# Kernel tuning notes

Hardware: AMD Instinct MI355X
Metric: run time of the kernel (lower is better)

The kernel has to match this reference:

```python
import jax, jax.numpy as jnp
import numpy as np

B, N = 128, 64
HID, MLP, DS, DV = 128, 128, 32, 32
DH = MLP - DS - DV  # 64
FILL = -10.0


def _embed_mask(x, W, b, fill):
    # Linear+ReLU on non-NaN rows; fill NaN rows with `fill` (matches embed_with_masking).
    nan = jnp.isnan(x).any(-1)
    e = jax.nn.relu(jnp.where(jnp.isnan(x), 0.0, x) @ W + b)
    return jnp.where(nan[..., None], jnp.asarray(fill, x.dtype), e)


def setup_inputs() -> dict:
    key = jax.random.key(0)
    ks = jax.random.split(key, 12)
    s = 0.05
    return {
        "hidden_states": jax.random.normal(ks[0], (B, N, HID), jnp.float32),
        "obs1": jax.random.normal(ks[1], (B, N, 2), jnp.float32),
        "obs2": jax.random.normal(ks[2], (B, N, 2), jnp.float32),
        "w_sp": jax.random.normal(ks[3], (2, DS), jnp.float32) * s,
        "b_sp": jnp.zeros((DS,), jnp.float32),
        "w_vel": jax.random.normal(ks[4], (2, DV), jnp.float32) * s,
        "b_vel": jnp.zeros((DV,), jnp.float32),
        "w_hid": jax.random.normal(ks[5], (HID, DH), jnp.float32) * s,
        "b_hid": jnp.zeros((DH,), jnp.float32),
        "wq": jax.random.normal(ks[6], (MLP, MLP), jnp.float32) * s,
        "wk": jax.random.normal(ks[7], (MLP, MLP), jnp.float32) * s,
        "wv": jax.random.normal(ks[8], (MLP, MLP), jnp.float32) * s,
        "in_proj_w": jax.random.normal(ks[9], (MLP, 3 * MLP), jnp.float32) * s,
        "in_proj_b": jnp.zeros((3 * MLP,), jnp.float32),
        "mha_out_w": jax.random.normal(ks[10], (MLP, MLP), jnp.float32) * s,
        "mha_out_b": jnp.zeros((MLP,), jnp.float32),
        "out_w": jax.random.normal(ks[11], (MLP, MLP), jnp.float32) * s,
        "out_b": jnp.zeros((MLP,), jnp.float32),
    }


def reference(hidden_states, obs1, obs2, w_sp, b_sp, w_vel, b_vel, w_hid, b_hid,
              wq, wk, wv, in_proj_w, in_proj_b, mha_out_w, mha_out_b, out_w, out_b):
    b, n = obs2.shape[0], obs2.shape[1]
    # relative positions: rel[b,i,j] = obs2[b,j] - obs2[b,i]
    rel = obs2[:, None, :, :] - obs2[:, :, None, :]              # [B,N,N,2]
    sp = _embed_mask(rel, w_sp, b_sp, FILL)                      # [B,N,N,DS]
    hid = _embed_mask(hidden_states, w_hid, b_hid, 0.0)          # [B,N,DH]
    hid_unf = jnp.broadcast_to(hid[:, None, :, :], (b, n, n, DH))
    vel = obs2 - obs1
    relvel = vel[:, None, :, :] - vel[:, :, None, :]             # [B,N,N,2]
    dv = _embed_mask(relvel * 4, w_vel, b_vel, FILL)             # [B,N,N,DV]
    emb = jnp.concatenate([sp, hid_unf, dv], axis=-1)            # [B,N,N,MLP]

    # MHA (1 head) in-proj weights split (stored as [in,out])
    w_iq, w_ik, w_iv = in_proj_w[:, :MLP], in_proj_w[:, MLP:2 * MLP], in_proj_w[:, 2 * MLP:]
    b_iq, b_ik, b_iv = in_proj_b[:MLP], in_proj_b[MLP:2 * MLP], in_proj_b[2 * MLP:]

    # Only the diagonal query position is kept by the final eye-mask gather,
    # and softmax rows are independent, so compute q only at j == i.
    idx = jnp.arange(n)
    emb_diag = emb[:, idx, idx]                                  # [B,N,MLP]
    q = (emb_diag @ wq) @ w_iq + b_iq                            # [B,N,MLP]
    k = (emb @ wk) @ w_ik + b_ik                                 # [B,N,N,MLP]
    v = (emb @ wv) @ w_iv + b_iv                                 # [B,N,N,MLP]

    scores = jnp.einsum('bid,bijd->bij', q, k) / jnp.sqrt(jnp.asarray(MLP, q.dtype))
    attn = jax.nn.softmax(scores, axis=-1)                       # [B,N,N]
    ctx = jnp.einsum('bij,bijd->bid', attn, v)                   # [B,N,MLP]
    mha_out = ctx @ mha_out_w + mha_out_b
    out = mha_out @ out_w + out_b                                # [B,N,out_dim]
    return out.reshape(b * n, -1)
```

## Files before the change

### kernel.cpp

```cpp
#include <hip/hip_runtime.h>

#define WS_WQC  0
#define WS_WKC  16384
#define WS_WVC  32768
#define WS_MOW  49152
#define WS_G    65536
#define WS_GS   69632
#define WS_GD   71680
#define WS_G0   73728
#define WS_GS0  73792
#define WS_GD0  73824
#define WS_FSP  73856
#define WS_FDV  77952
#define WS_FHID 82048
#define WS_FB   90240

__global__ __launch_bounds__(128) void precompute1(
    const float* __restrict__ wq, const float* __restrict__ wk,
    const float* __restrict__ wv, const float* __restrict__ in_proj_w,
    const float* __restrict__ mha_out_w, const float* __restrict__ out_w,
    float* __restrict__ ws)
{
    __shared__ float arow[128];
    const int mat = blockIdx.x & 3;
    const int r   = blockIdx.x >> 2;
    const int tid = threadIdx.x;
    const float* A; const float* Bm; int ldb; float* C;
    if (mat == 0)      { A = wq;        Bm = in_proj_w;       ldb = 384; C = ws + WS_WQC; }
    else if (mat == 1) { A = wk;        Bm = in_proj_w + 128; ldb = 384; C = ws + WS_WKC; }
    else if (mat == 2) { A = wv;        Bm = in_proj_w + 256; ldb = 384; C = ws + WS_WVC; }
    else               { A = mha_out_w; Bm = out_w;           ldb = 128; C = ws + WS_MOW; }
    arow[tid] = A[r * 128 + tid];
    __syncthreads();
    float acc = 0.f;
    #pragma unroll 8
    for (int d = 0; d < 128; ++d) acc = fmaf(arow[d], Bm[d * ldb + tid], acc);
    C[r * 128 + tid] = acc;
}

__global__ __launch_bounds__(128) void precompute2(
    const float* __restrict__ b_sp, const float* __restrict__ b_vel,
    const float* __restrict__ in_proj_b, const float* __restrict__ mha_out_b,
    const float* __restrict__ out_w, const float* __restrict__ out_b,
    float* __restrict__ ws)
{
    const float* Wqc = ws + WS_WQC;
    const float* Wkc = ws + WS_WKC;
    const float* Wvc = ws + WS_WVC;
    const float* Mow = ws + WS_MOW;
    const int bid = blockIdx.x, tid = threadIdx.x;
    __shared__ float sa[256];

    if (bid < 64) {
        const int r = bid;
        sa[tid] = Wqc[(32 + r) * 128 + tid];
        __syncthreads();
        const float* brow; float* dst;
        if (tid < 64)      { brow = Wkc + (32 + tid) * 128;      dst = ws + WS_G  + r * 64 + tid; }
        else if (tid < 96) { brow = Wkc + (tid - 64) * 128;      dst = ws + WS_GS + r * 32 + (tid - 64); }
        else               { brow = Wkc + (96 + tid - 96) * 128; dst = ws + WS_GD + r * 32 + (tid - 96); }
        float acc = 0.f;
        #pragma unroll 8
        for (int d = 0; d < 128; ++d) acc = fmaf(sa[d], brow[d], acc);
        *dst = acc;
    } else if (bid < 96) {
        const int s = bid - 64;
        sa[tid]       = Wvc[s * 128 + tid];
        sa[128 + tid] = Wvc[(96 + s) * 128 + tid];
        __syncthreads();
        float a1 = 0.f, a2 = 0.f;
        #pragma unroll 8
        for (int m = 0; m < 128; ++m) {
            const float mo = Mow[m * 128 + tid];
            a1 = fmaf(sa[m], mo, a1);
            a2 = fmaf(sa[128 + m], mo, a2);
        }
        ws[WS_FSP + s * 128 + tid] = a1;
        ws[WS_FDV + s * 128 + tid] = a2;
    } else if (bid < 160) {
        const int c = bid - 96;
        sa[tid] = Wvc[(32 + c) * 128 + tid];
        __syncthreads();
        float acc = 0.f;
        #pragma unroll 8
        for (int m = 0; m < 128; ++m) acc = fmaf(sa[m], Mow[m * 128 + tid], acc);
        ws[WS_FHID + c * 128 + tid] = acc;
    } else if (bid == 160) {
        float acc = out_b[tid];
        #pragma unroll 8
        for (int m = 0; m < 128; ++m) {
            acc = fmaf(in_proj_b[256 + m], Mow[m * 128 + tid], acc);
            acc = fmaf(mha_out_b[m], out_w[m * 128 + tid], acc);
        }
        ws[WS_FB + tid] = acc;
    } else {
        float qc = in_proj_b[tid];
        #pragma unroll 4
        for (int s = 0; s < 32; ++s) {
            qc = fmaf(fmaxf(b_sp[s], 0.f),  Wqc[s * 128 + tid], qc);
            qc = fmaf(fmaxf(b_vel[s], 0.f), Wqc[(96 + s) * 128 + tid], qc);
        }
        sa[tid] = qc;
        __syncthreads();
        const float* brow; float* dst;
        if (tid < 64)      { brow = Wkc + (32 + tid) * 128;      dst = ws + WS_G0  + tid; }
        else if (tid < 96) { brow = Wkc + (tid - 64) * 128;      dst = ws + WS_GS0 + (tid - 64); }
        else               { brow = Wkc + (96 + tid - 96) * 128; dst = ws + WS_GD0 + (tid - 96); }
        float acc = 0.f;
        #pragma unroll 8
        for (int d = 0; d < 128; ++d) acc = fmaf(sa[d], brow[d], acc);
        *dst = acc;
    }
}

__global__ __launch_bounds__(256) void attn_main(
    const float* __restrict__ hs, const float* __restrict__ obs1,
    const float* __restrict__ obs2,
    const float* __restrict__ w_sp, const float* __restrict__ b_sp,
    const float* __restrict__ w_vel, const float* __restrict__ b_vel,
    const float* __restrict__ w_hid, const float* __restrict__ b_hid,
    const float* __restrict__ ws, float* __restrict__ out)
{
    const int tid  = threadIdx.x;
    const int lane = tid & 63;
    const int b    = blockIdx.x >> 1;
    const int i0   = (blockIdx.x & 1) * 32;

    const float* Gm   = ws + WS_G;
    const float* Gs   = ws + WS_GS;
    const float* Gd   = ws + WS_GD;
    const float* g0v  = ws + WS_G0;
    const float* gs0v = ws + WS_GS0;
    const float* gd0v = ws + WS_GD0;
    const float* Fsp  = ws + WS_FSP;
    const float* Fdv  = ws + WS_FDV;
    const float* Fhid = ws + WS_FHID;
    const float* fbv  = ws + WS_FB;

    __shared__ __align__(16) float sA[8192];
    __shared__ __align__(16) float s_hid[4096];
    __shared__ __align__(16) float s_w[192];
    __shared__ __align__(16) float s_obs[256];

    float* const s_t    = sA;
    float* const s_qs   = sA + 2048;
    float* const s_qd   = sA + 3072;
    float* const s_hidT = sA + 4096;
    float* const s_ssp  = sA + 4096;
    float* const s_sdv  = sA + 5120;
    float* const s_ah   = sA + 6144;

    if (tid < 192) {
        float v;
        if (tid < 64)       v = w_sp[tid];
        else if (tid < 128) v = w_vel[tid - 64];
        else if (tid < 160) v = b_sp[tid - 128];
        else                v = b_vel[tid - 160];
        s_w[tid] = v;
    }
    if (tid < 64) {
        const int g = b * 64 + tid;
        const float ox = obs2[g * 2 + 0];
        const float oy = obs2[g * 2 + 1];
        const float vx = ox - obs1[g * 2 + 0];
        const float vy = oy - obs1[g * 2 + 1];
        *(float4*)&s_obs[tid * 4] = make_float4(ox, oy, vx, vy);
    }

    for (int h = 0; h < 2; ++h) {
        const float4* srcH = (const float4*)(hs + b * 8192 + h * 4096);
        float4* dstA = (float4*)sA;
        #pragma unroll
        for (int k = tid; k < 1024; k += 256) dstA[k] = srcH[k];
        __syncthreads();
        {
            const int ty = tid >> 4, tx = tid & 15;
            float a0c[4] = {0,0,0,0}, a1c[4] = {0,0,0,0};
            for (int d0 = 0; d0 < 128; d0 += 4) {
                const float4 a0 = *(const float4*)&sA[(2*ty+0)*128 + d0];
                const float4 a1 = *(const float4*)&sA[(2*ty+1)*128 + d0];
                const float* a0p = (const float*)&a0;
                const float* a1p = (const float*)&a1;
                #pragma unroll
                for (int dd = 0; dd < 4; ++dd) {
                    const float4 w4 = *(const float4*)&w_hid[(d0+dd)*64 + 4*tx];
                    a0c[0] = fmaf(a0p[dd], w4.x, a0c[0]);
                    a0c[1] = fmaf(a0p[dd], w4.y, a0c[1]);
                    a0c[2] = fmaf(a0p[dd], w4.z, a0c[2]);
                    a0c[3] = fmaf(a0p[dd], w4.w, a0c[3]);
                    a1c[0] = fmaf(a1p[dd], w4.x, a1c[0]);
                    a1c[1] = fmaf(a1p[dd], w4.y, a1c[1]);
                    a1c[2] = fmaf(a1p[dd], w4.z, a1c[2]);
                    a1c[3] = fmaf(a1p[dd], w4.w, a1c[3]);
                }
            }
            const float4 bh = *(const float4*)&b_hid[4*tx];
            float v0[4], v1[4];
            v0[0] = fmaxf(a0c[0] + bh.x, 0.f); v0[1] = fmaxf(a0c[1] + bh.y, 0.f);
            v0[2] = fmaxf(a0c[2] + bh.z, 0.f); v0[3] = fmaxf(a0c[3] + bh.w, 0.f);
            v1[0] = fmaxf(a1c[0] + bh.x, 0.f); v1[1] = fmaxf(a1c[1] + bh.y, 0.f);
            v1[2] = fmaxf(a1c[2] + bh.z, 0.f); v1[3] = fmaxf(a1c[3] + bh.w, 0.f);
            const int r0 = 32*h + 2*ty;
            *(float4*)&s_hid[(r0+0)*64 + 4*tx] = make_float4(v0[0], v0[1], v0[2], v0[3]);
            *(float4*)&s_hid[(r0+1)*64 + 4*tx] = make_float4(v1[0], v1[1], v1[2], v1[3]);
            #pragma unroll
            for (int cc = 0; cc < 4; ++cc)
                *(float2*)&s_hidT[(4*tx+cc)*64 + r0] = make_float2(v0[cc], v1[cc]);
        }
        __syncthreads();
    }

    {
        const int ty = tid >> 4, tx = tid & 15;
        const int r0 = i0 + 2*ty;
        {
            const float4 gb = *(const float4*)&g0v[4*tx];
            float t0[4] = {gb.x, gb.y, gb.z, gb.w};
            float t1[4] = {gb.x, gb.y, gb.z, gb.w};
            for (int k0 = 0; k0 < 64; k0 += 4) {
                const float4 a0 = *(const float4*)&s_hid[(r0+0)*64 + k0];
                const float4 a1 = *(const float4*)&s_hid[(r0+1)*64 + k0];
                const float* a0p = (const float*)&a0;
                const float* a1p = (const float*)&a1;
                #pragma unroll
                for (int kk = 0; kk < 4; ++kk) {
                    const float4 g4 = *(const float4*)&Gm[(k0+kk)*64 + 4*tx];
                    t0[0] = fmaf(a0p[kk], g4.x, t0[0]); t0[1] = fmaf(a0p[kk], g4.y, t0[1]);
                    t0[2] = fmaf(a0p[kk], g4.z, t0[2]); t0[3] = fmaf(a0p[kk], g4.w, t0[3]);
                    t1[0] = fmaf(a1p[kk], g4.x, t1[0]); t1[1] = fmaf(a1p[kk], g4.y, t1[1]);
                    t1[2] = fmaf(a1p[kk], g4.z, t1[2]); t1[3] = fmaf(a1p[kk], g4.w, t1[3]);
                }
            }
            *(float4*)&s_t[(2*ty+0)*64 + 4*tx] = make_float4(t0[0], t0[1], t0[2], t0[3]);
            *(float4*)&s_t[(2*ty+1)*64 + 4*tx] = make_float4(t1[0], t1[1], t1[2], t1[3]);
        }
        {
            const float* Bm  = (tx < 8) ? Gs : Gd;
            const float* bm0 = (tx < 8) ? gs0v : gd0v;
            float* dstm      = (tx < 8) ? s_qs : s_qd;
            const int nc = (tx & 7) * 4;
            const float4 bb = *(const float4*)&bm0[nc];
            float q0[4] = {bb.x, bb.y, bb.z, bb.w};
            float q1[4] = {bb.x, bb.y, bb.z, bb.w};
            for (int k0 = 0; k0 < 64; k0 += 4) {
                const float4 a0 = *(const float4*)&s_hid[(r0+0)*64 + k0];
                const float4 a1 = *(const float4*)&s_hid[(r0+1)*64 + k0];
                const float* a0p = (const float*)&a0;
                const float* a1p = (const float*)&a1;
                #pragma unroll
                for (int kk = 0; kk < 4; ++kk) {
                    const float4 g4 = *(const float4*)&Bm[(k0+kk)*32 + nc];
                    q0[0] = fmaf(a0p[kk], g4.x, q0[0]); q0[1] = fmaf(a0p[kk], g4.y, q0[1]);
                    q0[2] = fmaf(a0p[kk], g4.z, q0[2]); q0[3] = fmaf(a0p[kk], g4.w, q0[3]);
                    q1[0] = fmaf(a1p[kk], g4.x, q1[0]); q1[1] = fmaf(a1p[kk], g4.y, q1[1]);
                    q1[2] = fmaf(a1p[kk], g4.z, q1[2]); q1[3] = fmaf(a1p[kk], g4.w, q1[3]);
                }
            }
            *(float4*)&dstm[(2*ty+0)*32 + nc] = make_float4(q0[0], q0[1], q0[2], q0[3]);
            *(float4*)&dstm[(2*ty+1)*32 + nc] = make_float4(q1[0], q1[1], q1[2], q1[3]);
        }
    }
    __syncthreads();

    {
        const int ty = tid >> 4, tx = tid & 15;
        float q0[4] = {0,0,0,0}, q1[4] = {0,0,0,0};
        for (int c0 = 0; c0 < 64; c0 += 4) {
            const float4 t40 = *(const float4*)&s_t[(2*ty+0)*64 + c0];
            const float4 t41 = *(const float4*)&s_t[(2*ty+1)*64 + c0];
            const float* t0p = (const float*)&t40;
            const float* t1p = (const float*)&t41;
            #pragma unroll
            for (int cc = 0; cc < 4; ++cc) {
                const float4 h4 = *(const float4*)&s_hidT[(c0+cc)*64 + 4*tx];
                q0[0] = fmaf(t0p[cc], h4.x, q0[0]); q0[1] = fmaf(t0p[cc], h4.y, q0[1]);
                q0[2] = fmaf(t0p[cc], h4.z, q0[2]); q0[3] = fmaf(t0p[cc], h4.w, q0[3]);
                q1[0] = fmaf(t1p[cc], h4.x, q1[0]); q1[1] = fmaf(t1p[cc], h4.y, q1[1]);
                q1[2] = fmaf(t1p[cc], h4.z, q1[2]); q1[3] = fmaf(t1p[cc], h4.w, q1[3]);
            }
        }
        __syncthreads();
        *(float4*)&s_t[(2*ty+0)*64 + 4*tx] = make_float4(q0[0], q0[1], q0[2], q0[3]);
        *(float4*)&s_t[(2*ty+1)*64 + 4*tx] = make_float4(q1[0], q1[1], q1[2], q1[3]);
    }
    __syncthreads();

    {
        const int wid = tid >> 6;
        float relx[8], rely[8], dvx[8], dvy[8], accr[8];
        const float4 oj = *(const float4*)&s_obs[lane * 4];
        #pragma unroll
        for (int k = 0; k < 8; ++k) {
            const int i = i0 + wid * 8 + k;
            const float4 oi = *(const float4*)&s_obs[i * 4];
            relx[k] = oj.x - oi.x;
            rely[k] = oj.y - oi.y;
            dvx[k]  = (oj.z - oi.z) * 4.f;
            dvy[k]  = (oj.w - oi.w) * 4.f;
            accr[k] = 0.f;
        }
        for (int s0 = 0; s0 < 32; s0 += 4) {
            const float4 w0  = *(const float4*)&s_w[s0];
            const float4 w1  = *(const float4*)&s_w[32 + s0];
            const float4 wv0 = *(const float4*)&s_w[64 + s0];
            const float4 wv1 = *(const float4*)&s_w[96 + s0];
            const float4 bs  = *(const float4*)&s_w[128 + s0];
            const float4 bv  = *(const float4*)&s_w[160 + s0];
            #pragma unroll
            for (int k = 0; k < 8; ++k) {
                const int r = wid * 8 + k;
                const float4 qs4 = *(const float4*)&s_qs[r * 32 + s0];
                const float4 qd4 = *(const float4*)&s_qd[r * 32 + s0];
                float acc = accr[k];
                acc = fmaf(qs4.x, fmaxf(fmaf(relx[k], w0.x, fmaf(rely[k], w1.x, bs.x)), 0.f), acc);
                acc = fmaf(qs4.y, fmaxf(fmaf(relx[k], w0.y, fmaf(rely[k], w1.y, bs.y)), 0.f), acc);
                acc = fmaf(qs4.z, fmaxf(fmaf(relx[k], w0.z, fmaf(rely[k], w1.z, bs.z)), 0.f), acc);
                acc = fmaf(qs4.w, fmaxf(fmaf(relx[k], w0.w, fmaf(rely[k], w1.w, bs.w)), 0.f), acc);
                acc = fmaf(qd4.x, fmaxf(fmaf(dvx[k], wv0.x, fmaf(dvy[k], wv1.x, bv.x)), 0.f), acc);
                acc = fmaf(qd4.y, fmaxf(fmaf(dvx[k], wv0.y, fmaf(dvy[k], wv1.y, bv.y)), 0.f), acc);
                acc = fmaf(qd4.z, fmaxf(fmaf(dvx[k], wv0.z, fmaf(dvy[k], wv1.z, bv.z)), 0.f), acc);
                acc = fmaf(qd4.w, fmaxf(fmaf(dvx[k], wv0.w, fmaf(dvy[k], wv1.w, bv.w)), 0.f), acc);
                accr[k] = acc;
            }
        }
        const float scale = 0.08838834764831845f;
        #pragma unroll
        for (int k = 0; k < 8; ++k) {
            const int r = wid * 8 + k;
            const float sc = (s_t[r * 64 + lane] + accr[k]) * scale;
            float m = sc;
            #pragma unroll
            for (int off = 32; off > 0; off >>= 1) m = fmaxf(m, __shfl_xor(m, off, 64));
            const float e = __expf(sc - m);
            float sum = e;
            #pragma unroll
            for (int off = 32; off > 0; off >>= 1) sum += __shfl_xor(sum, off, 64);
            s_t[r * 64 + lane] = e / sum;
        }
    }
    __syncthreads();

    {
        const int sx = tid & 7, r6 = tid >> 3;
        const int i = i0 + r6;
        const float4 w0  = *(const float4*)&s_w[4*sx];
        const float4 w1  = *(const float4*)&s_w[32 + 4*sx];
        const float4 wv0 = *(const float4*)&s_w[64 + 4*sx];
        const float4 wv1 = *(const float4*)&s_w[96 + 4*sx];
        const float4 bs  = *(const float4*)&s_w[128 + 4*sx];
        const float4 bv  = *(const float4*)&s_w[160 + 4*sx];
        const float4 oi  = *(const float4*)&s_obs[i * 4];
        float sp0=0, sp1=0, sp2=0, sp3=0, dv0=0, dv1=0, dv2=0, dv3=0;
        for (int j0 = 0; j0 < 64; j0 += 4) {
            const float4 at4 = *(const float4*)&s_t[r6 * 64 + j0];
            const float* atp = (const float*)&at4;
            #pragma unroll
            for (int jj = 0; jj < 4; ++jj) {
                const float4 oj4 = *(const float4*)&s_obs[(j0 + jj) * 4];
                const float a  = atp[jj];
                const float rx = oj4.x - oi.x, ry = oj4.y - oi.y;
                const float dx = (oj4.z - oi.z) * 4.f, dy = (oj4.w - oi.w) * 4.f;
                sp0 = fmaf(a, fmaxf(fmaf(rx, w0.x, fmaf(ry, w1.x, bs.x)), 0.f), sp0);
                sp1 = fmaf(a, fmaxf(fmaf(rx, w0.y, fmaf(ry, w1.y, bs.y)), 0.f), sp1);
                sp2 = fmaf(a, fmaxf(fmaf(rx, w0.z, fmaf(ry, w1.z, bs.z)), 0.f), sp2);
                sp3 = fmaf(a, fmaxf(fmaf(rx, w0.w, fmaf(ry, w1.w, bs.w)), 0.f), sp3);
                dv0 = fmaf(a, fmaxf(fmaf(dx, wv0.x, fmaf(dy, wv1.x, bv.x)), 0.f), dv0);
                dv1 = fmaf(a, fmaxf(fmaf(dx, wv0.y, fmaf(dy, wv1.y, bv.y)), 0.f), dv1);
                dv2 = fmaf(a, fmaxf(fmaf(dx, wv0.z, fmaf(dy, wv1.z, bv.z)), 0.f), dv2);
                dv3 = fmaf(a, fmaxf(fmaf(dx, wv0.w, fmaf(dy, wv1.w, bv.w)), 0.f), dv3);
            }
        }
        *(float4*)&s_ssp[r6 * 32 + 4*sx] = make_float4(sp0, sp1, sp2, sp3);
        *(float4*)&s_sdv[r6 * 32 + 4*sx] = make_float4(dv0, dv1, dv2, dv3);

        const int ty = tid >> 4, tx = tid & 15;
        float h0[4] = {0,0,0,0}, h1[4] = {0,0,0,0};
        for (int j0 = 0; j0 < 64; j0 += 4) {
            const float4 at0 = *(const float4*)&s_t[(2*ty+0)*64 + j0];
            const float4 at1 = *(const float4*)&s_t[(2*ty+1)*64 + j0];
            const float* a0p = (const float*)&at0;
            const float* a1p = (const float*)&at1;
            #pragma unroll
            for (int jj = 0; jj < 4; ++jj) {
                const float4 h4 = *(const float4*)&s_hid[(j0+jj)*64 + 4*tx];
                h0[0] = fmaf(a0p[jj], h4.x, h0[0]); h0[1] = fmaf(a0p[jj], h4.y, h0[1]);
                h0[2] = fmaf(a0p[jj], h4.z, h0[2]); h0[3] = fmaf(a0p[jj], h4.w, h0[3]);
                h1[0] = fmaf(a1p[jj], h4.x, h1[0]); h1[1] = fmaf(a1p[jj], h4.y, h1[1]);
                h1[2] = fmaf(a1p[jj], h4.z, h1[2]); h1[3] = fmaf(a1p[jj], h4.w, h1[3]);
            }
        }
        *(float4*)&s_ah[(2*ty+0)*64 + 4*tx] = make_float4(h0[0], h0[1], h0[2], h0[3]);
        *(float4*)&s_ah[(2*ty+1)*64 + 4*tx] = make_float4(h1[0], h1[1], h1[2], h1[3]);
    }
    __syncthreads();

    {
        const int ty = tid >> 4, tx = tid & 15;
        const float4 fba = *(const float4*)&fbv[8*tx];
        const float4 fbb = *(const float4*)&fbv[8*tx + 4];
        float o0a[4] = {fba.x, fba.y, fba.z, fba.w};
        float o0b[4] = {fbb.x, fbb.y, fbb.z, fbb.w};
        float o1a[4] = {fba.x, fba.y, fba.z, fba.w};
        float o1b[4] = {fbb.x, fbb.y, fbb.z, fbb.w};

        #define ACC_TERM(SMAT, LD, FMAT, KMAX)                                        \
        for (int k0 = 0; k0 < (KMAX); k0 += 4) {                                      \
            const float4 a0 = *(const float4*)&SMAT[(2*ty+0)*(LD) + k0];              \
            const float4 a1 = *(const float4*)&SMAT[(2*ty+1)*(LD) + k0];              \
            const float* a0p = (const float*)&a0;                                     \
            const float* a1p = (const float*)&a1;                                     \
            _Pragma("unroll")                                                         \
            for (int kk = 0; kk < 4; ++kk) {                                          \
                const float4 fa = *(const float4*)&FMAT[(k0+kk)*128 + 8*tx];          \
                const float4 fbq = *(const float4*)&FMAT[(k0+kk)*128 + 8*tx + 4];     \
                o0a[0] = fmaf(a0p[kk], fa.x, o0a[0]); o0a[1] = fmaf(a0p[kk], fa.y, o0a[1]); \
                o0a[2] = fmaf(a0p[kk], fa.z, o0a[2]); o0a[3] = fmaf(a0p[kk], fa.w, o0a[3]); \
                o0b[0] = fmaf(a0p[kk], fbq.x, o0b[0]); o0b[1] = fmaf(a0p[kk], fbq.y, o0b[1]); \
                o0b[2] = fmaf(a0p[kk], fbq.z, o0b[2]); o0b[3] = fmaf(a0p[kk], fbq.w, o0b[3]); \
                o1a[0] = fmaf(a1p[kk], fa.x, o1a[0]); o1a[1] = fmaf(a1p[kk], fa.y, o1a[1]); \
                o1a[2] = fmaf(a1p[kk], fa.z, o1a[2]); o1a[3] = fmaf(a1p[kk], fa.w, o1a[3]); \
                o1b[0] = fmaf(a1p[kk], fbq.x, o1b[0]); o1b[1] = fmaf(a1p[kk], fbq.y, o1b[1]); \
                o1b[2] = fmaf(a1p[kk], fbq.z, o1b[2]); o1b[3] = fmaf(a1p[kk], fbq.w, o1b[3]); \
            }                                                                         \
        }
        ACC_TERM(s_ssp, 32, Fsp, 32)
        ACC_TERM(s_sdv, 32, Fdv, 32)
        ACC_TERM(s_ah,  64, Fhid, 64)
        #undef ACC_TERM

        const int gr = (b * 64 + i0 + 2*ty) * 128;
        *(float4*)&out[gr + 8*tx]       = make_float4(o0a[0], o0a[1], o0a[2], o0a[3]);
        *(float4*)&out[gr + 8*tx + 4]   = make_float4(o0b[0], o0b[1], o0b[2], o0b[3]);
        *(float4*)&out[gr + 128 + 8*tx]     = make_float4(o1a[0], o1a[1], o1a[2], o1a[3]);
        *(float4*)&out[gr + 128 + 8*tx + 4] = make_float4(o1b[0], o1b[1], o1b[2], o1b[3]);
    }
}

extern "C" void kernel_launch(void* const* d_in, const int* in_sizes, int n_in,
                              void* d_out, int out_size, void* d_ws, size_t ws_size,
                              hipStream_t stream) {
    const float* hs        = (const float*)d_in[0];
    const float* obs1      = (const float*)d_in[1];
    const float* obs2      = (const float*)d_in[2];
    const float* w_sp      = (const float*)d_in[3];
    const float* b_sp      = (const float*)d_in[4];
    const float* w_vel     = (const float*)d_in[5];
    const float* b_vel     = (const float*)d_in[6];
    const float* w_hid     = (const float*)d_in[7];
    const float* b_hid     = (const float*)d_in[8];
    const float* wq        = (const float*)d_in[9];
    const float* wk        = (const float*)d_in[10];
    const float* wv        = (const float*)d_in[11];
    const float* in_proj_w = (const float*)d_in[12];
    const float* in_proj_b = (const float*)d_in[13];
    const float* mha_out_w = (const float*)d_in[14];
    const float* mha_out_b = (const float*)d_in[15];
    const float* out_w     = (const float*)d_in[16];
    const float* out_b     = (const float*)d_in[17];
    float* ws  = (float*)d_ws;
    float* out = (float*)d_out;

    precompute1<<<512, 128, 0, stream>>>(wq, wk, wv, in_proj_w, mha_out_w, out_w, ws);
    precompute2<<<162, 128, 0, stream>>>(b_sp, b_vel, in_proj_b, mha_out_b, out_w, out_b, ws);
    attn_main<<<256, 256, 0, stream>>>(hs, obs1, obs2, w_sp, b_sp, w_vel, b_vel,
                                       w_hid, b_hid, ws, out);
}
```

Baseline: 141.0 us.

## Split attention over more blocks, precompute hidden embedding, pad shared memory

Doubles the attention grid to four blocks per batch, each handling 16 query rows, so more CUs are busy. When the workspace is large enough, the hidden-state embedding is computed once per batch in precompute1 and reused from workspace, rather than being recomputed by every attention block. Shared-memory rows are padded (68/36/132 strides) to reduce bank conflicts, and the combined Wk matrix is stored transposed for coalesced reads in precompute2. The cost is an extra global round-trip for the hidden embedding and less per-thread register reuse from the smaller row tiles.

```diff
diff --git a/kernel.cpp b/kernel.cpp
--- a/kernel.cpp
+++ b/kernel.cpp
@@ -1,41 +1,84 @@
 #include <hip/hip_runtime.h>
 
-#define WS_WQC  0
-#define WS_WKC  16384
-#define WS_WVC  32768
-#define WS_MOW  49152
-#define WS_G    65536
-#define WS_GS   69632
-#define WS_GD   71680
-#define WS_G0   73728
-#define WS_GS0  73792
-#define WS_GD0  73824
-#define WS_FSP  73856
-#define WS_FDV  77952
-#define WS_FHID 82048
-#define WS_FB   90240
-
-__global__ __launch_bounds__(128) void precompute1(
+#define WS_WQC   0
+#define WS_WKCT  16384
+#define WS_WVC   32768
+#define WS_MOW   49152
+#define WS_G     65536
+#define WS_GS    69632
+#define WS_GD    71680
+#define WS_G0    73728
+#define WS_GS0   73792
+#define WS_GD0   73824
+#define WS_FSP   73856
+#define WS_FDV   77952
+#define WS_FHID  82048
+#define WS_FB    90240
+#define WS_HID   90368
+#define WS_NEED_HID_BYTES ((size_t)(90368 + 128*64*64) * 4)
+
+__global__ __launch_bounds__(256) void precompute1(
     const float* __restrict__ wq, const float* __restrict__ wk,
     const float* __restrict__ wv, const float* __restrict__ in_proj_w,
     const float* __restrict__ mha_out_w, const float* __restrict__ out_w,
-    float* __restrict__ ws)
+    const float* __restrict__ hs, const float* __restrict__ w_hid,
+    const float* __restrict__ b_hid, float* __restrict__ ws)
 {
-    __shared__ float arow[128];
-    const int mat = blockIdx.x & 3;
-    const int r   = blockIdx.x >> 2;
+    __shared__ __align__(16) float sbuf[4224];
     const int tid = threadIdx.x;
-    const float* A; const float* Bm; int ldb; float* C;
-    if (mat == 0)      { A = wq;        Bm = in_proj_w;       ldb = 384; C = ws + WS_WQC; }
-    else if (mat == 1) { A = wk;        Bm = in_proj_w + 128; ldb = 384; C = ws + WS_WKC; }
-    else if (mat == 2) { A = wv;        Bm = in_proj_w + 256; ldb = 384; C = ws + WS_WVC; }
-    else               { A = mha_out_w; Bm = out_w;           ldb = 128; C = ws + WS_MOW; }
-    arow[tid] = A[r * 128 + tid];
-    __syncthreads();
-    float acc = 0.f;
-    #pragma unroll 8
-    for (int d = 0; d < 128; ++d) acc = fmaf(arow[d], Bm[d * ldb + tid], acc);
-    C[r * 128 + tid] = acc;
+
+    if (blockIdx.x < 256) {
+        const int mat  = blockIdx.x >> 6;
+        const int rp   = blockIdx.x & 63;
+        const int rsel = tid >> 7;
+        const int col  = tid & 127;
+        const int r    = 2 * rp + rsel;
+        const float* A; const float* Bm; int ldb;
+        if (mat == 0)      { A = wq;        Bm = in_proj_w;       ldb = 384; }
+        else if (mat == 1) { A = wk;        Bm = in_proj_w + 128; ldb = 384; }
+        else if (mat == 2) { A = wv;        Bm = in_proj_w + 256; ldb = 384; }
+        else               { A = mha_out_w; Bm = out_w;           ldb = 128; }
+        sbuf[tid] = A[r * 128 + col];
+        __syncthreads();
+        float acc = 0.f;
+        #pragma unroll 8
+        for (int d = 0; d < 128; ++d) acc = fmaf(sbuf[rsel * 128 + d], Bm[d * ldb + col], acc);
+        if (mat == 0)      ws[WS_WQC  + r * 128 + col] = acc;
+        else if (mat == 1) ws[WS_WKCT + col * 128 + r] = acc;
+        else if (mat == 2) ws[WS_WVC  + r * 128 + col] = acc;
+        else               ws[WS_MOW  + r * 128 + col] = acc;
+    } else {
+        const int b2 = blockIdx.x - 256;
+        const int b = b2 >> 1, half = b2 & 1;
+        const float4* src = (const float4*)(hs + b * 8192 + half * 4096);
+        for (int k = tid; k < 1024; k += 256) {
+            const int row = k >> 5, c = k & 31;
+            *(float4*)&sbuf[row * 132 + 4 * c] = src[k];
+        }
+        __syncthreads();
+        const int ty = tid >> 4, tx = tid & 15;
+        float a0c[4] = {0,0,0,0}, a1c[4] = {0,0,0,0};
+        for (int d0 = 0; d0 < 128; d0 += 4) {
+            const float4 a0 = *(const float4*)&sbuf[(2*ty+0)*132 + d0];
+            const float4 a1 = *(const float4*)&sbuf[(2*ty+1)*132 + d0];
+            const float* a0p = (const float*)&a0;
+            const float* a1p = (const float*)&a1;
+            #pragma unroll
+            for (int dd = 0; dd < 4; ++dd) {
+                const float4 w4 = *(const float4*)&w_hid[(d0+dd)*64 + 4*tx];
+                a0c[0] = fmaf(a0p[dd], w4.x, a0c[0]); a0c[1] = fmaf(a0p[dd], w4.y, a0c[1]);
+                a0c[2] = fmaf(a0p[dd], w4.z, a0c[2]); a0c[3] = fmaf(a0p[dd], w4.w, a0c[3]);
+                a1c[0] = fmaf(a1p[dd], w4.x, a1c[0]); a1c[1] = fmaf(a1p[dd], w4.y, a1c[1]);
+                a1c[2] = fmaf(a1p[dd], w4.z, a1c[2]); a1c[3] = fmaf(a1p[dd], w4.w, a1c[3]);
+            }
+        }
+        const float4 bh = *(const float4*)&b_hid[4*tx];
+        float* dst = ws + WS_HID + b * 4096 + (32*half + 2*ty) * 64 + 4*tx;
+        *(float4*)dst        = make_float4(fmaxf(a0c[0]+bh.x,0.f), fmaxf(a0c[1]+bh.y,0.f),
+                                           fmaxf(a0c[2]+bh.z,0.f), fmaxf(a0c[3]+bh.w,0.f));
+        *(float4*)(dst + 64) = make_float4(fmaxf(a1c[0]+bh.x,0.f), fmaxf(a1c[1]+bh.y,0.f),
+                                           fmaxf(a1c[2]+bh.z,0.f), fmaxf(a1c[3]+bh.w,0.f));
+    }
 }
 
 __global__ __launch_bounds__(128) void precompute2(
@@ -44,10 +87,10 @@
     const float* __restrict__ out_w, const float* __restrict__ out_b,
     float* __restrict__ ws)
 {
-    const float* Wqc = ws + WS_WQC;
-    const float* Wkc = ws + WS_WKC;
-    const float* Wvc = ws + WS_WVC;
-    const float* Mow = ws + WS_MOW;
+    const float* Wqc  = ws + WS_WQC;
+    const float* WkcT = ws + WS_WKCT;
+    const float* Wvc  = ws + WS_WVC;
+    const float* Mow  = ws + WS_MOW;
     const int bid = blockIdx.x, tid = threadIdx.x;
     __shared__ float sa[256];
 
@@ -55,13 +98,13 @@
         const int r = bid;
         sa[tid] = Wqc[(32 + r) * 128 + tid];
         __syncthreads();
-        const float* brow; float* dst;
-        if (tid < 64)      { brow = Wkc + (32 + tid) * 128;      dst = ws + WS_G  + r * 64 + tid; }
-        else if (tid < 96) { brow = Wkc + (tid - 64) * 128;      dst = ws + WS_GS + r * 32 + (tid - 64); }
-        else               { brow = Wkc + (96 + tid - 96) * 128; dst = ws + WS_GD + r * 32 + (tid - 96); }
+        const int colIdx = (tid < 64) ? 32 + tid : ((tid < 96) ? tid - 64 : tid);
+        float* dst = (tid < 64) ? ws + WS_G  + r * 64 + tid
+                   : (tid < 96) ? ws + WS_GS + r * 32 + (tid - 64)
+                                : ws + WS_GD + r * 32 + (tid - 96);
         float acc = 0.f;
         #pragma unroll 8
-        for (int d = 0; d < 128; ++d) acc = fmaf(sa[d], brow[d], acc);
+        for (int d = 0; d < 128; ++d) acc = fmaf(sa[d], WkcT[d * 128 + colIdx], acc);
         *dst = acc;
     } else if (bid < 96) {
         const int s = bid - 64;
@@ -102,17 +145,30 @@
         }
         sa[tid] = qc;
         __syncthreads();
-        const float* brow; float* dst;
-        if (tid < 64)      { brow = Wkc + (32 + tid) * 128;      dst = ws + WS_G0  + tid; }
-        else if (tid < 96) { brow = Wkc + (tid - 64) * 128;      dst = ws + WS_GS0 + (tid - 64); }
-        else               { brow = Wkc + (96 + tid - 96) * 128; dst = ws + WS_GD0 + (tid - 96); }
+        const int colIdx = (tid < 64) ? 32 + tid : ((tid < 96) ? tid - 64 : tid);
+        float* dst = (tid < 64) ? ws + WS_G0  + tid
+                   : (tid < 96) ? ws + WS_GS0 + (tid - 64)
+                                : ws + WS_GD0 + (tid - 96);
         float acc = 0.f;
         #pragma unroll 8
-        for (int d = 0; d < 128; ++d) acc = fmaf(sa[d], brow[d], acc);
+        for (int d = 0; d < 128; ++d) acc = fmaf(sa[d], WkcT[d * 128 + colIdx], acc);
         *dst = acc;
     }
 }
 
+#define L_T    0
+#define L_SC   1088
+#define L_QS   2176
+#define L_QD   2752
+#define L_SSP  3328
+#define L_SDV  3904
+#define L_AH   4480
+#define L_HID  5568
+#define L_HIDT 9920
+#define L_OBS  14272
+#define L_W    14528
+
+template <bool HIDWS>
 __global__ __launch_bounds__(256) void attn_main(
     const float* __restrict__ hs, const float* __restrict__ obs1,
     const float* __restrict__ obs2,
@@ -123,8 +179,8 @@
 {
     const int tid  = threadIdx.x;
     const int lane = tid & 63;
-    const int b    = blockIdx.x >> 1;
-    const int i0   = (blockIdx.x & 1) * 32;
+    const int b    = blockIdx.x >> 2;
+    const int i0   = (blockIdx.x & 3) * 16;
 
     const float* Gm   = ws + WS_G;
     const float* Gs   = ws + WS_GS;
@@ -137,18 +193,19 @@
     const float* Fhid = ws + WS_FHID;
     const float* fbv  = ws + WS_FB;
 
-    __shared__ __align__(16) float sA[8192];
-    __shared__ __align__(16) float s_hid[4096];
-    __shared__ __align__(16) float s_w[192];
-    __shared__ __align__(16) float s_obs[256];
-
-    float* const s_t    = sA;
-    float* const s_qs   = sA + 2048;
-    float* const s_qd   = sA + 3072;
-    float* const s_hidT = sA + 4096;
-    float* const s_ssp  = sA + 4096;
-    float* const s_sdv  = sA + 5120;
-    float* const s_ah   = sA + 6144;
+    __shared__ __align__(16) float smem[14720];
+    float* const s_t    = smem + L_T;
+    float* const s_sc   = smem + L_SC;
+    float* const s_qs   = smem + L_QS;
+    float* const s_qd   = smem + L_QD;
+    float* const s_ssp  = smem + L_SSP;
+    float* const s_sdv  = smem + L_SDV;
+    float* const s_ah   = smem + L_AH;
+    float* const s_hid  = smem + L_HID;
+    float* const s_hidT = smem + L_HIDT;
+    float* const s_obs  = smem + L_OBS;
+    float* const s_w    = smem + L_W;
+    float* const s_hs   = smem;
 
     if (tid < 192) {
         float v;
@@ -167,131 +224,111 @@
         *(float4*)&s_obs[tid * 4] = make_float4(ox, oy, vx, vy);
     }
 
-    for (int h = 0; h < 2; ++h) {
-        const float4* srcH = (const float4*)(hs + b * 8192 + h * 4096);
-        float4* dstA = (float4*)sA;
-        #pragma unroll
-        for (int k = tid; k < 1024; k += 256) dstA[k] = srcH[k];
-        __syncthreads();
-        {
+    if (HIDWS) {
+        const float4* src = (const float4*)(ws + WS_HID + b * 4096);
+        for (int k = tid; k < 1024; k += 256) {
+            const int row = k >> 4, c4 = (k & 15) * 4;
+            const float4 v = src[k];
+            *(float4*)&s_hid[row * 68 + c4] = v;
+            s_hidT[(c4 + 0) * 68 + row] = v.x;
+            s_hidT[(c4 + 1) * 68 + row] = v.y;
+            s_hidT[(c4 + 2) * 68 + row] = v.z;
+            s_hidT[(c4 + 3) * 68 + row] = v.w;
+        }
+        __syncthreads();
+    } else {
+        for (int h = 0; h < 2; ++h) {
+            const float4* srcH = (const float4*)(hs + b * 8192 + h * 4096);
+            for (int k = tid; k < 1024; k += 256) {
+                const int row = k >> 5, c = k & 31;
+                *(float4*)&s_hs[row * 132 + 4 * c] = srcH[k];
+            }
+            __syncthreads();
             const int ty = tid >> 4, tx = tid & 15;
             float a0c[4] = {0,0,0,0}, a1c[4] = {0,0,0,0};
             for (int d0 = 0; d0 < 128; d0 += 4) {
-                const float4 a0 = *(const float4*)&sA[(2*ty+0)*128 + d0];
-                const float4 a1 = *(const float4*)&sA[(2*ty+1)*128 + d0];
+                const float4 a0 = *(const float4*)&s_hs[(2*ty+0)*132 + d0];
+                const float4 a1 = *(const float4*)&s_hs[(2*ty+1)*132 + d0];
                 const float* a0p = (const float*)&a0;
                 const float* a1p = (const float*)&a1;
                 #pragma unroll
                 for (int dd = 0; dd < 4; ++dd) {
                     const float4 w4 = *(const float4*)&w_hid[(d0+dd)*64 + 4*tx];
-                    a0c[0] = fmaf(a0p[dd], w4.x, a0c[0]);
-                    a0c[1] = fmaf(a0p[dd], w4.y, a0c[1]);
-                    a0c[2] = fmaf(a0p[dd], w4.z, a0c[2]);
-                    a0c[3] = fmaf(a0p[dd], w4.w, a0c[3]);
-                    a1c[0] = fmaf(a1p[dd], w4.x, a1c[0]);
-                    a1c[1] = fmaf(a1p[dd], w4.y, a1c[1]);
-                    a1c[2] = fmaf(a1p[dd], w4.z, a1c[2]);
-                    a1c[3] = fmaf(a1p[dd], w4.w, a1c[3]);
+                    a0c[0] = fmaf(a0p[dd], w4.x, a0c[0]); a0c[1] = fmaf(a0p[dd], w4.y, a0c[1]);
+                    a0c[2] = fmaf(a0p[dd], w4.z, a0c[2]); a0c[3] = fmaf(a0p[dd], w4.w, a0c[3]);
+                    a1c[0] = fmaf(a1p[dd], w4.x, a1c[0]); a1c[1] = fmaf(a1p[dd], w4.y, a1c[1]);
+                    a1c[2] = fmaf(a1p[dd], w4.z, a1c[2]); a1c[3] = fmaf(a1p[dd], w4.w, a1c[3]);
                 }
             }
             const float4 bh = *(const float4*)&b_hid[4*tx];
             float v0[4], v1[4];
-            v0[0] = fmaxf(a0c[0] + bh.x, 0.f); v0[1] = fmaxf(a0c[1] + bh.y, 0.f);
-            v0[2] = fmaxf(a0c[2] + bh.z, 0.f); v0[3] = fmaxf(a0c[3] + bh.w, 0.f);
-            v1[0] = fmaxf(a1c[0] + bh.x, 0.f); v1[1] = fmaxf(a1c[1] + bh.y, 0.f);
-            v1[2] = fmaxf(a1c[2] + bh.z, 0.f); v1[3] = fmaxf(a1c[3] + bh.w, 0.f);
+            v0[0]=fmaxf(a0c[0]+bh.x,0.f); v0[1]=fmaxf(a0c[1]+bh.y,0.f);
+            v0[2]=fmaxf(a0c[2]+bh.z,0.f); v0[3]=fmaxf(a0c[3]+bh.w,0.f);
+            v1[0]=fmaxf(a1c[0]+bh.x,0.f); v1[1]=fmaxf(a1c[1]+bh.y,0.f);
+            v1[2]=fmaxf(a1c[2]+bh.z,0.f); v1[3]=fmaxf(a1c[3]+bh.w,0.f);
             const int r0 = 32*h + 2*ty;
-            *(float4*)&s_hid[(r0+0)*64 + 4*tx] = make_float4(v0[0], v0[1], v0[2], v0[3]);
-            *(float4*)&s_hid[(r0+1)*64 + 4*tx] = make_float4(v1[0], v1[1], v1[2], v1[3]);
+            *(float4*)&s_hid[(r0+0)*68 + 4*tx] = make_float4(v0[0],v0[1],v0[2],v0[3]);
+            *(float4*)&s_hid[(r0+1)*68 + 4*tx] = make_float4(v1[0],v1[1],v1[2],v1[3]);
             #pragma unroll
             for (int cc = 0; cc < 4; ++cc)
-                *(float2*)&s_hidT[(4*tx+cc)*64 + r0] = make_float2(v0[cc], v1[cc]);
-        }
-        __syncthreads();
+                *(float2*)&s_hidT[(4*tx+cc)*68 + r0] = make_float2(v0[cc], v1[cc]);
+            __syncthreads();
+        }
     }
 
     {
         const int ty = tid >> 4, tx = tid & 15;
-        const int r0 = i0 + 2*ty;
-        {
-            const float4 gb = *(const float4*)&g0v[4*tx];
-            float t0[4] = {gb.x, gb.y, gb.z, gb.w};
-            float t1[4] = {gb.x, gb.y, gb.z, gb.w};
-            for (int k0 = 0; k0 < 64; k0 += 4) {
-                const float4 a0 = *(const float4*)&s_hid[(r0+0)*64 + k0];
-                const float4 a1 = *(const float4*)&s_hid[(r0+1)*64 + k0];
-                const float* a0p = (const float*)&a0;
-                const float* a1p = (const float*)&a1;
-                #pragma unroll
-                for (int kk = 0; kk < 4; ++kk) {
-                    const float4 g4 = *(const float4*)&Gm[(k0+kk)*64 + 4*tx];
-                    t0[0] = fmaf(a0p[kk], g4.x, t0[0]); t0[1] = fmaf(a0p[kk], g4.y, t0[1]);
-                    t0[2] = fmaf(a0p[kk], g4.z, t0[2]); t0[3] = fmaf(a0p[kk], g4.w, t0[3]);
-                    t1[0] = fmaf(a1p[kk], g4.x, t1[0]); t1[1] = fmaf(a1p[kk], g4.y, t1[1]);
-                    t1[2] = fmaf(a1p[kk], g4.z, t1[2]); t1[3] = fmaf(a1p[kk], g4.w, t1[3]);
-                }
-            }
-            *(float4*)&s_t[(2*ty+0)*64 + 4*tx] = make_float4(t0[0], t0[1], t0[2], t0[3]);
-            *(float4*)&s_t[(2*ty+1)*64 + 4*tx] = make_float4(t1[0], t1[1], t1[2], t1[3]);
-        }
-        {
-            const float* Bm  = (tx < 8) ? Gs : Gd;
-            const float* bm0 = (tx < 8) ? gs0v : gd0v;
-            float* dstm      = (tx < 8) ? s_qs : s_qd;
-            const int nc = (tx & 7) * 4;
-            const float4 bb = *(const float4*)&bm0[nc];
-            float q0[4] = {bb.x, bb.y, bb.z, bb.w};
-            float q1[4] = {bb.x, bb.y, bb.z, bb.w};
-            for (int k0 = 0; k0 < 64; k0 += 4) {
-                const float4 a0 = *(const float4*)&s_hid[(r0+0)*64 + k0];
-                const float4 a1 = *(const float4*)&s_hid[(r0+1)*64 + k0];
-                const float* a0p = (const float*)&a0;
-                const float* a1p = (const float*)&a1;
-                #pragma unroll
-                for (int kk = 0; kk < 4; ++kk) {
-                    const float4 g4 = *(const float4*)&Bm[(k0+kk)*32 + nc];
-                    q0[0] = fmaf(a0p[kk], g4.x, q0[0]); q0[1] = fmaf(a0p[kk], g4.y, q0[1]);
-                    q0[2] = fmaf(a0p[kk], g4.z, q0[2]); q0[3] = fmaf(a0p[kk], g4.w, q0[3]);
-                    q1[0] = fmaf(a1p[kk], g4.x, q1[0]); q1[1] = fmaf(a1p[kk], g4.y, q1[1]);
-                    q1[2] = fmaf(a1p[kk], g4.z, q1[2]); q1[3] = fmaf(a1p[kk], g4.w, q1[3]);
-                }
-            }
-            *(float4*)&dstm[(2*ty+0)*32 + nc] = make_float4(q0[0], q0[1], q0[2], q0[3]);
-            *(float4*)&dstm[(2*ty+1)*32 + nc] = make_float4(q1[0], q1[1], q1[2], q1[3]);
-        }
+        const int r = i0 + ty;
+        const float* Bq  = (tx < 8) ? Gs : Gd;
+        const float* bq0 = (tx < 8) ? gs0v : gd0v;
+        float* dstq      = (tx < 8) ? s_qs : s_qd;
+        const int nc = (tx & 7) * 4;
+        const float4 gb = *(const float4*)&g0v[4*tx];
+        const float4 qb = *(const float4*)&bq0[nc];
+        float aT[4] = {gb.x, gb.y, gb.z, gb.w};
+        float aQ[4] = {qb.x, qb.y, qb.z, qb.w};
+        for (int k0 = 0; k0 < 64; k0 += 4) {
+            const float4 a = *(const float4*)&s_hid[r * 68 + k0];
+            const float* ap = (const float*)&a;
+            #pragma unroll
+            for (int kk = 0; kk < 4; ++kk) {
+                const float4 g4 = *(const float4*)&Gm[(k0+kk)*64 + 4*tx];
+                const float4 q4 = *(const float4*)&Bq[(k0+kk)*32 + nc];
+                aT[0] = fmaf(ap[kk], g4.x, aT[0]); aT[1] = fmaf(ap[kk], g4.y, aT[1]);
+                aT[2] = fmaf(ap[kk], g4.z, aT[2]); aT[3] = fmaf(ap[kk], g4.w, aT[3]);
+                aQ[0] = fmaf(ap[kk], q4.x, aQ[0]); aQ[1] = fmaf(ap[kk], q4.y, aQ[1]);
+                aQ[2] = fmaf(ap[kk], q4.z, aQ[2]); aQ[3] = fmaf(ap[kk], q4.w, aQ[3]);
+            }
+        }
+        *(float4*)&s_t[ty * 68 + 4*tx] = make_float4(aT[0], aT[1], aT[2], aT[3]);
+        *(float4*)&dstq[ty * 36 + nc]  = make_float4(aQ[0], aQ[1], aQ[2], aQ[3]);
     }
     __syncthreads();
 
     {
         const int ty = tid >> 4, tx = tid & 15;
-        float q0[4] = {0,0,0,0}, q1[4] = {0,0,0,0};
+        float q[4] = {0,0,0,0};
         for (int c0 = 0; c0 < 64; c0 += 4) {
-            const float4 t40 = *(const float4*)&s_t[(2*ty+0)*64 + c0];
-            const float4 t41 = *(const float4*)&s_t[(2*ty+1)*64 + c0];
-            const float* t0p = (const float*)&t40;
-            const float* t1p = (const float*)&t41;
+            const float4 t4 = *(const float4*)&s_t[ty * 68 + c0];
+            const float* tp = (const float*)&t4;
             #pragma unroll
             for (int cc = 0; cc < 4; ++cc) {
-                const float4 h4 = *(const float4*)&s_hidT[(c0+cc)*64 + 4*tx];
-                q0[0] = fmaf(t0p[cc], h4.x, q0[0]); q0[1] = fmaf(t0p[cc], h4.y, q0[1]);
-                q0[2] = fmaf(t0p[cc], h4.z, q0[2]); q0[3] = fmaf(t0p[cc], h4.w, q0[3]);
-                q1[0] = fmaf(t1p[cc], h4.x, q1[0]); q1[1] = fmaf(t1p[cc], h4.y, q1[1]);
-                q1[2] = fmaf(t1p[cc], h4.z, q1[2]); q1[3] = fmaf(t1p[cc], h4.w, q1[3]);
-            }
-        }
-        __syncthreads();
-        *(float4*)&s_t[(2*ty+0)*64 + 4*tx] = make_float4(q0[0], q0[1], q0[2], q0[3]);
-        *(float4*)&s_t[(2*ty+1)*64 + 4*tx] = make_float4(q1[0], q1[1], q1[2], q1[3]);
+                const float4 h4 = *(const float4*)&s_hidT[(c0+cc)*68 + 4*tx];
+                q[0] = fmaf(tp[cc], h4.x, q[0]); q[1] = fmaf(tp[cc], h4.y, q[1]);
+                q[2] = fmaf(tp[cc], h4.z, q[2]); q[3] = fmaf(tp[cc], h4.w, q[3]);
+            }
+        }
+        *(float4*)&s_sc[ty * 68 + 4*tx] = make_float4(q[0], q[1], q[2], q[3]);
     }
     __syncthreads();
 
     {
         const int wid = tid >> 6;
-        float relx[8], rely[8], dvx[8], dvy[8], accr[8];
+        float relx[4], rely[4], dvx[4], dvy[4], accr[4];
         const float4 oj = *(const float4*)&s_obs[lane * 4];
         #pragma unroll
-        for (int k = 0; k < 8; ++k) {
-            const int i = i0 + wid * 8 + k;
+        for (int k = 0; k < 4; ++k) {
+            const int i = i0 + wid * 4 + k;
             const float4 oi = *(const float4*)&s_obs[i * 4];
             relx[k] = oj.x - oi.x;
             rely[k] = oj.y - oi.y;
@@ -307,10 +344,10 @@
             const float4 bs  = *(const float4*)&s_w[128 + s0];
             const float4 bv  = *(const float4*)&s_w[160 + s0];
             #pragma unroll
-            for (int k = 0; k < 8; ++k) {
-                const int r = wid * 8 + k;
-                const float4 qs4 = *(const float4*)&s_qs[r * 32 + s0];
-                const float4 qd4 = *(const float4*)&s_qd[r * 32 + s0];
+            for (int k = 0; k < 4; ++k) {
+                const int r = wid * 4 + k;
+                const float4 qs4 = *(const float4*)&s_qs[r * 36 + s0];
+                const float4 qd4 = *(const float4*)&s_qd[r * 36 + s0];
                 float acc = accr[k];
                 acc = fmaf(qs4.x, fmaxf(fmaf(relx[k], w0.x, fmaf(rely[k], w1.x, bs.x)), 0.f), acc);
                 acc = fmaf(qs4.y, fmaxf(fmaf(relx[k], w0.y, fmaf(rely[k], w1.y, bs.y)), 0.f), acc);
@@ -325,9 +362,9 @@
         }
         const float scale = 0.08838834764831845f;
         #pragma unroll
-        for (int k = 0; k < 8; ++k) {
-            const int r = wid * 8 + k;
-            const float sc = (s_t[r * 64 + lane] + accr[k]) * scale;
+        for (int k = 0; k < 4; ++k) {
+            const int r = wid * 4 + k;
+            const float sc = (s_sc[r * 68 + lane] + accr[k]) * scale;
             float m = sc;
             #pragma unroll
             for (int off = 32; off > 0; off >>= 1) m = fmaxf(m, __shfl_xor(m, off, 64));
@@ -335,62 +372,52 @@
             float sum = e;
             #pragma unroll
             for (int off = 32; off > 0; off >>= 1) sum += __shfl_xor(sum, off, 64);
-            s_t[r * 64 + lane] = e / sum;
+            s_sc[r * 68 + lane] = e / sum;
         }
     }
     __syncthreads();
 
     {
-        const int sx = tid & 7, r6 = tid >> 3;
+        const int r6 = tid >> 4, sx = tid & 15;
         const int i = i0 + r6;
-        const float4 w0  = *(const float4*)&s_w[4*sx];
-        const float4 w1  = *(const float4*)&s_w[32 + 4*sx];
-        const float4 wv0 = *(const float4*)&s_w[64 + 4*sx];
-        const float4 wv1 = *(const float4*)&s_w[96 + 4*sx];
-        const float4 bs  = *(const float4*)&s_w[128 + 4*sx];
-        const float4 bv  = *(const float4*)&s_w[160 + 4*sx];
-        const float4 oi  = *(const float4*)&s_obs[i * 4];
-        float sp0=0, sp1=0, sp2=0, sp3=0, dv0=0, dv1=0, dv2=0, dv3=0;
+        const bool isSp = (sx < 8);
+        const int nc = (sx & 7) * 4;
+        const float4 wA = *(const float4*)&s_w[(isSp ? 0 : 64) + nc];
+        const float4 wB = *(const float4*)&s_w[(isSp ? 32 : 96) + nc];
+        const float4 bb = *(const float4*)&s_w[(isSp ? 128 : 160) + nc];
+        const float4 oi = *(const float4*)&s_obs[i * 4];
+        float c0=0, c1=0, c2=0, c3=0;
         for (int j0 = 0; j0 < 64; j0 += 4) {
-            const float4 at4 = *(const float4*)&s_t[r6 * 64 + j0];
-            const float* atp = (const float*)&at4;
+            const float4 a4 = *(const float4*)&s_sc[r6 * 68 + j0];
+            const float* ap = (const float*)&a4;
             #pragma unroll
             for (int jj = 0; jj < 4; ++jj) {
                 const float4 oj4 = *(const float4*)&s_obs[(j0 + jj) * 4];
-                const float a  = atp[jj];
-                const float rx = oj4.x - oi.x, ry = oj4.y - oi.y;
-                const float dx = (oj4.z - oi.z) * 4.f, dy = (oj4.w - oi.w) * 4.f;
-                sp0 = fmaf(a, fmaxf(fmaf(rx, w0.x, fmaf(ry, w1.x, bs.x)), 0.f), sp0);
-                sp1 = fmaf(a, fmaxf(fmaf(rx, w0.y, fmaf(ry, w1.y, bs.y)), 0.f), sp1);
-                sp2 = fmaf(a, fmaxf(fmaf(rx, w0.z, fmaf(ry, w1.z, bs.z)), 0.f), sp2);
-                sp3 = fmaf(a, fmaxf(fmaf(rx, w0.w, fmaf(ry, w1.w, bs.w)), 0.f), sp3);
-                dv0 = fmaf(a, fmaxf(fmaf(dx, wv0.x, fmaf(dy, wv1.x, bv.x)), 0.f), dv0);
-                dv1 = fmaf(a, fmaxf(fmaf(dx, wv0.y, fmaf(dy, wv1.y, bv.y)), 0.f), dv1);
-                dv2 = fmaf(a, fmaxf(fmaf(dx, wv0.z, fmaf(dy, wv1.z, bv.z)), 0.f), dv2);
-                dv3 = fmaf(a, fmaxf(fmaf(dx, wv0.w, fmaf(dy, wv1.w, bv.w)), 0.f), dv3);
-            }
-        }
-        *(float4*)&s_ssp[r6 * 32 + 4*sx] = make_float4(sp0, sp1, sp2, sp3);
-        *(float4*)&s_sdv[r6 * 32 + 4*sx] = make_float4(dv0, dv1, dv2, dv3);
+                const float a = ap[jj];
+                const float ux = isSp ? (oj4.x - oi.x) : (oj4.z - oi.z) * 4.f;
+                const float uy = isSp ? (oj4.y - oi.y) : (oj4.w - oi.w) * 4.f;
+                c0 = fmaf(a, fmaxf(fmaf(ux, wA.x, fmaf(uy, wB.x, bb.x)), 0.f), c0);
+                c1 = fmaf(a, fmaxf(fmaf(ux, wA.y, fmaf(uy, wB.y, bb.y)), 0.f), c1);
+                c2 = fmaf(a, fmaxf(fmaf(ux, wA.z, fmaf(uy, wB.z, bb.z)), 0.f), c2);
+                c3 = fmaf(a, fmaxf(fmaf(ux, wA.w, fmaf(uy, wB.w, bb.w)), 0.f), c3);
+            }
+        }
+        float* dst = isSp ? (s_ssp + r6 * 36 + nc) : (s_sdv + r6 * 36 + nc);
+        *(float4*)dst = make_float4(c0, c1, c2, c3);
 
         const int ty = tid >> 4, tx = tid & 15;
-        float h0[4] = {0,0,0,0}, h1[4] = {0,0,0,0};
+        float h[4] = {0,0,0,0};
         for (int j0 = 0; j0 < 64; j0 += 4) {
-            const float4 at0 = *(const float4*)&s_t[(2*ty+0)*64 + j0];
-            const float4 at1 = *(const float4*)&s_t[(2*ty+1)*64 + j0];
-            const float* a0p = (const float*)&at0;
-            const float* a1p = (const float*)&at1;
+            const float4 at4 = *(const float4*)&s_sc[ty * 68 + j0];
+            const float* atp = (const float*)&at4;
             #pragma unroll
             for (int jj = 0; jj < 4; ++jj) {
-                const float4 h4 = *(const float4*)&s_hid[(j0+jj)*64 + 4*tx];
-                h0[0] = fmaf(a0p[jj], h4.x, h0[0]); h0[1] = fmaf(a0p[jj], h4.y, h0[1]);
-                h0[2] = fmaf(a0p[jj], h4.z, h0[2]); h0[3] = fmaf(a0p[jj], h4.w, h0[3]);
-                h1[0] = fmaf(a1p[jj], h4.x, h1[0]); h1[1] = fmaf(a1p[jj], h4.y, h1[1]);
-                h1[2] = fmaf(a1p[jj], h4.z, h1[2]); h1[3] = fmaf(a1p[jj], h4.w, h1[3]);
-            }
-        }
-        *(float4*)&s_ah[(2*ty+0)*64 + 4*tx] = make_float4(h0[0], h0[1], h0[2], h0[3]);
-        *(float4*)&s_ah[(2*ty+1)*64 + 4*tx] = make_float4(h1[0], h1[1], h1[2], h1[3]);
+                const float4 h4 = *(const float4*)&s_hid[(j0+jj)*68 + 4*tx];
+                h[0] = fmaf(atp[jj], h4.x, h[0]); h[1] = fmaf(atp[jj], h4.y, h[1]);
+                h[2] = fmaf(atp[jj], h4.z, h[2]); h[3] = fmaf(atp[jj], h4.w, h[3]);
+            }
+        }
+        *(float4*)&s_ah[ty * 68 + 4*tx] = make_float4(h[0], h[1], h[2], h[3]);
     }
     __syncthreads();
 
@@ -398,41 +425,31 @@
         const int ty = tid >> 4, tx = tid & 15;
         const float4 fba = *(const float4*)&fbv[8*tx];
         const float4 fbb = *(const float4*)&fbv[8*tx + 4];
-        float o0a[4] = {fba.x, fba.y, fba.z, fba.w};
-        float o0b[4] = {fbb.x, fbb.y, fbb.z, fbb.w};
-        float o1a[4] = {fba.x, fba.y, fba.z, fba.w};
-        float o1b[4] = {fbb.x, fbb.y, fbb.z, fbb.w};
+        float oa[4] = {fba.x, fba.y, fba.z, fba.w};
+        float ob[4] = {fbb.x, fbb.y, fbb.z, fbb.w};
 
         #define ACC_TERM(SMAT, LD, FMAT, KMAX)                                        \
         for (int k0 = 0; k0 < (KMAX); k0 += 4) {                                      \
-            const float4 a0 = *(const float4*)&SMAT[(2*ty+0)*(LD) + k0];              \
-            const float4 a1 = *(const float4*)&SMAT[(2*ty+1)*(LD) + k0];              \
-            const float* a0p = (const float*)&a0;                                     \
-            const float* a1p = (const float*)&a1;                                     \
+            const float4 a4 = *(const float4*)&SMAT[ty * (LD) + k0];                  \
+            const float* ap = (const float*)&a4;                                      \
             _Pragma("unroll")                                                         \
             for (int kk = 0; kk < 4; ++kk) {                                          \
                 const float4 fa = *(const float4*)&FMAT[(k0+kk)*128 + 8*tx];          \
-                const float4 fbq = *(const float4*)&FMAT[(k0+kk)*128 + 8*tx + 4];     \
-                o0a[0] = fmaf(a0p[kk], fa.x, o0a[0]); o0a[1] = fmaf(a0p[kk], fa.y, o0a[1]); \
-                o0a[2] = fmaf(a0p[kk], fa.z, o0a[2]); o0a[3] = fmaf(a0p[kk], fa.w, o0a[3]); \
-                o0b[0] = fmaf(a0p[kk], fbq.x, o0b[0]); o0b[1] = fmaf(a0p[kk], fbq.y, o0b[1]); \
-                o0b[2] = fmaf(a0p[kk], fbq.z, o0b[2]); o0b[3] = fmaf(a0p[kk], fbq.w, o0b[3]); \
-                o1a[0] = fmaf(a1p[kk], fa.x, o1a[0]); o1a[1] = fmaf(a1p[kk], fa.y, o1a[1]); \
-                o1a[2] = fmaf(a1p[kk], fa.z, o1a[2]); o1a[3] = fmaf(a1p[kk], fa.w, o1a[3]); \
-                o1b[0] = fmaf(a1p[kk], fbq.x, o1b[0]); o1b[1] = fmaf(a1p[kk], fbq.y, o1b[1]); \
-                o1b[2] = fmaf(a1p[kk], fbq.z, o1b[2]); o1b[3] = fmaf(a1p[kk], fbq.w, o1b[3]); \
+                const float4 fq = *(const float4*)&FMAT[(k0+kk)*128 + 8*tx + 4];      \
+                oa[0] = fmaf(ap[kk], fa.x, oa[0]); oa[1] = fmaf(ap[kk], fa.y, oa[1]); \
+                oa[2] = fmaf(ap[kk], fa.z, oa[2]); oa[3] = fmaf(ap[kk], fa.w, oa[3]); \
+                ob[0] = fmaf(ap[kk], fq.x, ob[0]); ob[1] = fmaf(ap[kk], fq.y, ob[1]); \
+                ob[2] = fmaf(ap[kk], fq.z, ob[2]); ob[3] = fmaf(ap[kk], fq.w, ob[3]); \
             }                                                                         \
         }
-        ACC_TERM(s_ssp, 32, Fsp, 32)
-        ACC_TERM(s_sdv, 32, Fdv, 32)
-        ACC_TERM(s_ah,  64, Fhid, 64)
+        ACC_TERM(s_ssp, 36, Fsp, 32)
+        ACC_TERM(s_sdv, 36, Fdv, 32)
+        ACC_TERM(s_ah,  68, Fhid, 64)
         #undef ACC_TERM
 
-        const int gr = (b * 64 + i0 + 2*ty) * 128;
-        *(float4*)&out[gr + 8*tx]       = make_float4(o0a[0], o0a[1], o0a[2], o0a[3]);
-        *(float4*)&out[gr + 8*tx + 4]   = make_float4(o0b[0], o0b[1], o0b[2], o0b[3]);
-        *(float4*)&out[gr + 128 + 8*tx]     = make_float4(o1a[0], o1a[1], o1a[2], o1a[3]);
-        *(float4*)&out[gr + 128 + 8*tx + 4] = make_float4(o1b[0], o1b[1], o1b[2], o1b[3]);
+        const int gr = (b * 64 + i0 + ty) * 128;
+        *(float4*)&out[gr + 8*tx]     = make_float4(oa[0], oa[1], oa[2], oa[3]);
+        *(float4*)&out[gr + 8*tx + 4] = make_float4(ob[0], ob[1], ob[2], ob[3]);
     }
 }
 
@@ -460,8 +477,17 @@
     float* ws  = (float*)d_ws;
     float* out = (float*)d_out;
 
-    precompute1<<<512, 128, 0, stream>>>(wq, wk, wv, in_proj_w, mha_out_w, out_w, ws);
-    precompute2<<<162, 128, 0, stream>>>(b_sp, b_vel, in_proj_b, mha_out_b, out_w, out_b, ws);
-    attn_main<<<256, 256, 0, stream>>>(hs, obs1, obs2, w_sp, b_sp, w_vel, b_vel,
-                                       w_hid, b_hid, ws, out);
+    const bool hidws = (ws_size >= WS_NEED_HID_BYTES);
+
+    precompute1<<<hidws ? 512 : 256, 256, 0, stream>>>(
+        wq, wk, wv, in_proj_w, mha_out_w, out_w, hs, w_hid, b_hid, ws);
+    precompute2<<<162, 128, 0, stream>>>(
+        b_sp, b_vel, in_proj_b, mha_out_b, out_w, out_b, ws);
+    if (hidws) {
+        attn_main<true><<<512, 256, 0, stream>>>(hs, obs1, obs2, w_sp, b_sp, w_vel, b_vel,
+                                                 w_hid, b_hid, ws, out);
+    } else {
+        attn_main<false><<<512, 256, 0, stream>>>(hs, obs1, obs2, w_sp, b_sp, w_vel, b_vel,
+                                                  w_hid, b_hid, ws, out);
+    }
 }
```

Measured after the change: 159.7 us. 1.13x slower.
